# Optimization experiments

Hardware: AMD Instinct MI355X
Metric: run time of the kernel (lower is better)

## Reference

```python
import jax, jax.numpy as jnp
import numpy as np

DEPTH = 2   # depth
H = 8       # heads
DH = 32     # dim_head
DIM = 256   # model dim (= H*DH)
W = 2       # sliding_window_size
C = 4       # compress_block_size == selection_block_size
NSEL = 2    # num_selected_blocks
B, S = 4, 2048


def layernorm(x, g, b, eps=1e-5):
    m = x.mean(-1, keepdims=True)
    v = jnp.var(x, axis=-1, keepdims=True)
    return (x - m) * jax.lax.rsqrt(v + eps) * g + b


def msoftmax(s, mask):
    # numerically-safe masked softmax; rows with no visible key output zeros
    s = jnp.where(mask, s, -1e9)
    p = jax.nn.softmax(s, axis=-1)
    return jnp.where(jnp.any(mask, axis=-1, keepdims=True), p, 0.0)


def nsa(x, Wq, Wk, Wv, Wg, Wo):
    # Native sparse attention: compressed + top-k selected blocks + sliding window,
    # combined with per-head sigmoid gates.
    b, s, d = x.shape
    nb = s // C
    q = (x @ Wq).reshape(b, s, H, DH).transpose(0, 2, 1, 3)  # [B,H,S,DH]
    k = (x @ Wk).reshape(b, s, H, DH).transpose(0, 2, 1, 3)
    v = (x @ Wv).reshape(b, s, H, DH).transpose(0, 2, 1, 3)
    scale = DH ** -0.5
    t = jnp.arange(s)

    # ---- compressed branch: mean-pooled KV blocks, causal over fully-past blocks
    kb = k.reshape(b, H, nb, C, DH)
    vb = v.reshape(b, H, nb, C, DH)
    kc = kb.mean(3)
    vc = vb.mean(3)
    sc = jnp.einsum('bhsd,bhnd->bhsn', q, kc) * scale       # [B,H,S,nb]
    blk_end = jnp.arange(nb) * C + (C - 1)
    cmask = blk_end[None, :] <= t[:, None]                   # [S,nb]
    pc = msoftmax(sc, cmask[None, None])
    oc = jnp.einsum('bhsn,bhnd->bhsd', pc, vc)

    # ---- selection branch: own block always + top (NSEL-1) blocks by compressed score
    own = t // C                                             # [S]
    not_own = jnp.arange(nb)[None, :] != own[:, None]        # [S,nb]
    sel_scores = jnp.where(not_own[None, None], pc, -1.0)
    top_idx = jax.lax.top_k(sel_scores, NSEL - 1)[1]         # [B,H,S,NSEL-1]
    own_idx = jnp.broadcast_to(own[None, None, :, None], (b, H, s, 1))
    idx = jnp.concatenate([own_idx, top_idx], axis=-1)       # [B,H,S,NSEL]
    idxf = idx.reshape(b, H, s * NSEL, 1, 1)
    sk = jnp.take_along_axis(kb, idxf, axis=2).reshape(b, H, s, NSEL * C, DH)
    sv = jnp.take_along_axis(vb, idxf, axis=2).reshape(b, H, s, NSEL * C, DH)
    pos = (idx[..., None] * C + jnp.arange(C)).reshape(b, H, s, NSEL * C)
    fmask = pos <= t[None, None, :, None]
    sf = jnp.einsum('bhsd,bhskd->bhsk', q, sk) * scale
    pf = msoftmax(sf, fmask)
    of = jnp.einsum('bhsk,bhskd->bhsd', pf, sv)

    # ---- sliding-window branch: causal local window of W tokens (incl. self)
    off = jnp.arange(W) - (W - 1)
    wpos = t[:, None] + off[None, :]                         # [S,W]
    widx = jnp.clip(wpos, 0, s - 1)
    kw = jnp.take(k, widx.reshape(-1), axis=2).reshape(b, H, s, W, DH)
    vw = jnp.take(v, widx.reshape(-1), axis=2).reshape(b, H, s, W, DH)
    sw = jnp.einsum('bhsd,bhsjd->bhsj', q, kw) * scale
    pw = msoftmax(sw, (wpos >= 0)[None, None])
    ow = jnp.einsum('bhsj,bhsjd->bhsd', pw, vw)

    # ---- gated combine + output projection
    g = jax.nn.sigmoid(x @ Wg).reshape(b, s, 3, H).transpose(0, 3, 1, 2)  # [B,H,S,3]
    o = g[..., 0:1] * oc + g[..., 1:2] * of + g[..., 2:3] * ow
    return o.transpose(0, 2, 1, 3).reshape(b, s, H * DH) @ Wo


def forward(x, ln_a_g, ln_a_b, Wq, Wk, Wv, Wg, Wo, ln_f_g, ln_f_b, W1, b1, W2, b2):
    for l in range(DEPTH):
        for j in range(2):  # two attention sub-layers per block
            i = l * 2 + j
            h = layernorm(x, ln_a_g[i], ln_a_b[i])
            x = x + nsa(h, Wq[i], Wk[i], Wv[i], Wg[i], Wo[i])
        h = layernorm(x, ln_f_g[l], ln_f_b[l])
        h = h @ W1[l] + b1[l]
        h = jnp.where(h > 0, h, 0.01 * h)  # LeakyReLU
        x = x + h @ W2[l] + b2[l]
    return x


def setup_inputs() -> dict:
    key = jax.random.key(0)
    ks = jax.random.split(key, 8)
    A = DEPTH * 2
    r = lambda k, shp: jax.random.normal(k, shp, jnp.float32) * 0.02
    return {
        'x': jax.random.normal(ks[0], (B, S, DIM), jnp.float32),
        'ln_a_g': jnp.ones((A, DIM), jnp.float32),
        'ln_a_b': jnp.zeros((A, DIM), jnp.float32),
        'Wq': r(ks[1], (A, DIM, H * DH)),
        'Wk': r(ks[2], (A, DIM, H * DH)),
        'Wv': r(ks[3], (A, DIM, H * DH)),
        'Wg': r(ks[4], (A, DIM, 3 * H)),
        'Wo': r(ks[5], (A, H * DH, DIM)),
        'ln_f_g': jnp.ones((DEPTH, DIM), jnp.float32),
        'ln_f_b': jnp.zeros((DEPTH, DIM), jnp.float32),
        'W1': r(ks[6], (DEPTH, DIM, 2 * DIM)),
        'b1': jnp.zeros((DEPTH, 2 * DIM), jnp.float32),
        'W2': r(ks[7], (DEPTH, 2 * DIM, DIM)),
        'b2': jnp.zeros((DEPTH, DIM), jnp.float32),
    }


def reference(x, ln_a_g, ln_a_b, Wq, Wk, Wv, Wg, Wo, ln_f_g, ln_f_b, W1, b1, W2, b2):
    return forward(x, ln_a_g, ln_a_b, Wq, Wk, Wv, Wg, Wo, ln_f_g, ln_f_b, W1, b1, W2, b2)
```

## Files before the change

### kernel.cpp

```cpp
#include <hip/hip_runtime.h>
#include <hip/hip_bf16.h>
#include <math.h>

#define NH 8
#define DH 32
#define DIM 256
#define SEQ 2048
#define BATCH 4
#define NB 512
#define QKS 512
#define VGS 320
#define SCALE 0.17677669529663687f

typedef short short8v __attribute__((ext_vector_type(8)));
typedef float float4v __attribute__((ext_vector_type(4)));

__device__ __forceinline__ float sigmoidf_(float x){ return 1.f/(1.f+__expf(-x)); }
__device__ __forceinline__ ushort f2bf(float f){
  uint b = __float_as_uint(f);
  return (ushort)((b + 0x7fffu + ((b>>16)&1u)) >> 16);
}
__device__ __forceinline__ float bf2f(ushort u){ return __uint_as_float(((uint)u)<<16); }
__device__ __forceinline__ float bflo(uint u){ return __uint_as_float(u<<16); }
__device__ __forceinline__ float bfhi(uint u){ return __uint_as_float(u & 0xffff0000u); }
__device__ __forceinline__ uint pk2(float a, float b){ return (uint)f2bf(a) | ((uint)f2bf(b)<<16); }
__device__ __forceinline__ void bfu4_to_f32(uint4 u, float* f){
  f[0]=bflo(u.x); f[1]=bfhi(u.x);
  f[2]=bflo(u.y); f[3]=bfhi(u.y);
  f[4]=bflo(u.z); f[5]=bfhi(u.z);
  f[6]=bflo(u.w); f[7]=bfhi(u.w);
}

__global__ void copy_f32(const float* __restrict__ in, float* __restrict__ out, int n4){
  int i = blockIdx.x*blockDim.x + threadIdx.x;
  if (i < n4) ((float4*)out)[i] = ((const float4*)in)[i];
}

__global__ void build_wqk(const float* __restrict__ Wq, const float* __restrict__ Wk, float* __restrict__ out){
  int i = blockIdx.x*256 + threadIdx.x;
  if (i >= 4*256*QKS) return;
  int col = i & 511, rk = (i>>9)&255, l = i>>17;
  out[i] = (col < 256) ? Wq[((size_t)l*256+rk)*256+col] : Wk[((size_t)l*256+rk)*256+col-256];
}
__global__ void build_wvgT(const float* __restrict__ Wv, const float* __restrict__ Wg, ushort* __restrict__ out){
  int i = blockIdx.x*256 + threadIdx.x;
  if (i >= 4*VGS*256) return;
  int k = i & 255, n = (i>>8)%VGS, l = i/(VGS*256);
  float v = 0.f;
  if      (n < 256) v = Wv[((size_t)l*256+k)*256+n];
  else if (n < 280) v = Wg[((size_t)l*256+k)*24 + (n-256)];
  out[i] = f2bf(v);
}
__global__ void build_wT(const float* __restrict__ in, ushort* __restrict__ out, int L, int K, int N){
  int i = blockIdx.x*256 + threadIdx.x;
  if (i >= L*K*N) return;
  int k = i % K, n = (i/K) % N, l = i/(K*N);
  out[i] = f2bf(in[((size_t)l*K+k)*N+n]);
}

__global__ __launch_bounds__(256) void ln_k(const float* __restrict__ x, const float* __restrict__ g,
                                            const float* __restrict__ b, float* __restrict__ h,
                                            ushort* __restrict__ hb){
  int row  = blockIdx.x*4 + (threadIdx.x>>6);
  int lane = threadIdx.x & 63;
  int c = lane*4;
  const float* xr = x + (size_t)row*DIM + c;
  float4 v = *(const float4*)xr;
  float s = v.x+v.y+v.z+v.w;
  float q = v.x*v.x+v.y*v.y+v.z*v.z+v.w*v.w;
  #pragma unroll
  for (int off=32; off>0; off>>=1){ s += __shfl_xor(s, off); q += __shfl_xor(q, off); }
  float mean = s * (1.f/DIM);
  float var  = q * (1.f/DIM) - mean*mean;
  float rs = rsqrtf(var + 1e-5f);
  float4 gg = *(const float4*)(g + c);
  float4 bb = *(const float4*)(b + c);
  float4 o;
  o.x = (v.x-mean)*rs*gg.x + bb.x;
  o.y = (v.y-mean)*rs*gg.y + bb.y;
  o.z = (v.z-mean)*rs*gg.z + bb.z;
  o.w = (v.w-mean)*rs*gg.w + bb.w;
  *(float4*)(h + (size_t)row*DIM + c) = o;
  uint2 u;
  u.x = pk2(o.x, o.y);
  u.y = pk2(o.z, o.w);
  *(uint2*)&hb[(size_t)row*DIM + c] = u;
}

template<bool BIAS, bool LEAKY, bool ACC>
__global__ __launch_bounds__(256) void gemm_f32(const float* __restrict__ A, const float* __restrict__ B,
                                                const float* __restrict__ bias, float* __restrict__ C,
                                                int M, int N, int K){
  __shared__ float As[32][132];
  __shared__ float Bs[32][68];
  int tid = threadIdx.x;
  int m0 = blockIdx.x*128, n0 = blockIdx.y*64;
  int tx = tid & 15, ty = tid >> 4;
  int ar = tid >> 1;
  int ac = (tid & 1)*16;
  int bk = tid >> 3;
  int bn = (tid & 7)*8;
  const float* Ap = A + (size_t)(m0+ar)*K + ac;
  const float* Bp = B + (size_t)bk*N + n0 + bn;
  float4 apre[4], bpre[2];
  #pragma unroll
  for (int j=0;j<4;j++) apre[j] = *(const float4*)(Ap + 4*j);
  bpre[0] = *(const float4*)Bp;
  bpre[1] = *(const float4*)(Bp + 4);
  float acc[8][4];
  #pragma unroll
  for (int i=0;i<8;i++)
    #pragma unroll
    for (int j=0;j<4;j++) acc[i][j]=0.f;
  for (int k0=0; k0<K; k0+=32){
    #pragma unroll
    for (int j=0;j<4;j++){
      As[ac+4*j+0][ar]=apre[j].x; As[ac+4*j+1][ar]=apre[j].y;
      As[ac+4*j+2][ar]=apre[j].z; As[ac+4*j+3][ar]=apre[j].w;
    }
    *(float4*)&Bs[bk][bn]   = bpre[0];
    *(float4*)&Bs[bk][bn+4] = bpre[1];
    __syncthreads();
    if (k0 + 32 < K){
      #pragma unroll
      for (int j=0;j<4;j++) apre[j] = *(const float4*)(Ap + k0 + 32 + 4*j);
      bpre[0] = *(const float4*)(Bp + (size_t)(k0+32)*N);
      bpre[1] = *(const float4*)(Bp + (size_t)(k0+32)*N + 4);
    }
    #pragma unroll
    for (int kk=0;kk<32;kk++){
      float4 bv  = *(const float4*)&Bs[kk][tx*4];
      float4 av0 = *(const float4*)&As[kk][ty*8];
      float4 av1 = *(const float4*)&As[kk][ty*8+4];
      float av[8] = {av0.x,av0.y,av0.z,av0.w,av1.x,av1.y,av1.z,av1.w};
      float bw[4] = {bv.x,bv.y,bv.z,bv.w};
      #pragma unroll
      for (int i=0;i<8;i++)
        #pragma unroll
        for (int j=0;j<4;j++) acc[i][j] += av[i]*bw[j];
    }
    __syncthreads();
  }
  #pragma unroll
  for (int i=0;i<8;i++){
    int m = m0 + ty*8 + i;
    #pragma unroll
    for (int j=0;j<4;j++){
      int n = n0 + tx*4 + j;
      float val = acc[i][j];
      if (BIAS)  val += bias[n];
      if (LEAKY) val = val > 0.f ? val : 0.01f*val;
      float* cp = C + (size_t)m*N + n;
      if (ACC) val += *cp;
      *cp = val;
    }
  }
}

template<bool BIAS, bool LEAKY, bool ACC, bool OBF16>
__global__ __launch_bounds__(256) void gemm_bf16(const ushort* __restrict__ A, const ushort* __restrict__ Bt,
                                                 const float* __restrict__ bias, void* __restrict__ Cv,
                                                 int M, int N, int K){
  __shared__ ushort Al[128*64];
  __shared__ ushort Bl[64*64];
  int tid = threadIdx.x;
  int m0 = blockIdx.x*128, n0 = blockIdx.y*64;
  int w = tid>>6, lane = tid&63;
  int wm = w>>1, wn = w&1;
  float4v acc[4][2];
  #pragma unroll
  for (int i=0;i<4;i++)
    #pragma unroll
    for (int j=0;j<2;j++) acc[i][j] = (float4v){0.f,0.f,0.f,0.f};
  for (int k0=0; k0<K; k0+=64){
    #pragma unroll
    for (int i=0;i<4;i++){
      int id = tid + 256*i;
      int r = id>>3, c = id&7;
      *(uint4*)&Al[r*64 + ((c ^ (r&7))*8)] = *(const uint4*)&A[(size_t)(m0+r)*K + k0 + c*8];
    }
    #pragma unroll
    for (int i=0;i<2;i++){
      int id = tid + 256*i;
      int r = id>>3, c = id&7;
      *(uint4*)&Bl[r*64 + ((c ^ (r&7))*8)] = *(const uint4*)&Bt[(size_t)(n0+r)*K + k0 + c*8];
    }
    __syncthreads();
    #pragma unroll
    for (int kk=0; kk<2; ++kk){
      short8v a[4], bfr[2];
      #pragma unroll
      for (int mf=0; mf<4; mf++){
        int r = wm*64 + mf*16 + (lane&15);
        int c = (kk*4 + (lane>>4)) ^ (r&7);
        a[mf] = *(short8v*)&Al[r*64 + c*8];
      }
      #pragma unroll
      for (int nf=0; nf<2; nf++){
        int r = wn*32 + nf*16 + (lane&15);
        int c = (kk*4 + (lane>>4)) ^ (r&7);
        bfr[nf] = *(short8v*)&Bl[r*64 + c*8];
      }
      #pragma unroll
      for (int mf=0; mf<4; mf++)
        #pragma unroll
        for (int nf=0; nf<2; nf++)
          acc[mf][nf] = __builtin_amdgcn_mfma_f32_16x16x32_bf16(a[mf], bfr[nf], acc[mf][nf], 0, 0, 0);
    }
    __syncthreads();
  }
  #pragma unroll
  for (int nf=0; nf<2; nf++){
    int col = n0 + wn*32 + nf*16 + (lane&15);
    float bv = BIAS ? bias[col] : 0.f;
    #pragma unroll
    for (int mf=0; mf<4; mf++){
      #pragma unroll
      for (int r=0; r<4; r++){
        int row = m0 + wm*64 + mf*16 + (lane>>4)*4 + r;
        float vv = acc[mf][nf][r];
        if (BIAS) vv += bv;
        if (LEAKY) vv = vv > 0.f ? vv : 0.01f*vv;
        if (OBF16) ((ushort*)Cv)[(size_t)row*N + col] = f2bf(vv);
        else {
          float* C = (float*)Cv;
          if (ACC) vv += C[(size_t)row*N + col];
          C[(size_t)row*N + col] = vv;
        }
      }
    }
  }
}

__global__ void pool_k(const float* __restrict__ qk, const ushort* __restrict__ vg,
                       float* __restrict__ kc, ushort* __restrict__ vc){
  int i = blockIdx.x*256 + threadIdx.x;
  if (i >= BATCH*NH*NB*DH) return;
  int d = i & 31, n = (i >> 5) & 511, h = (i >> 14) & 7, b = i >> 17;
  size_t kb = ((size_t)(b*SEQ + n*4))*QKS + 256 + h*DH + d;
  kc[i] = 0.25f*(qk[kb] + qk[kb+QKS] + qk[kb+2*QKS] + qk[kb+3*QKS]);
  size_t vb = ((size_t)(b*SEQ + n*4))*VGS + h*DH + d;
  vc[i] = f2bf(0.25f*(bf2f(vg[vb]) + bf2f(vg[vb+VGS]) + bf2f(vg[vb+2*VGS]) + bf2f(vg[vb+3*VGS])));
}

__global__ __launch_bounds__(256, 4) void nsa_attn(
    const float* __restrict__ qk, const ushort* __restrict__ vg,
    const float* __restrict__ kc, const ushort* __restrict__ vc,
    ushort* __restrict__ o)
{
  __shared__ float  kt[64*32];
  __shared__ ushort vt[64*32];
  __shared__ ushort accs[4*64*32];
  __shared__ float4 meta[4*64];
  int e = blockIdx.x;
  int hh = e & 7;
  int b  = (e >> 3) & 3;
  int qq = (e >> 5) & 7;
  int r  = e >> 8;
  int g  = (r==0) ? (31-qq) : (r==1) ? qq : (r==2) ? (23-qq) : (8+qq);
  int tid = threadIdx.x;
  int w = tid >> 6, lane = tid & 63;
  const float*  kcg = kc + ((size_t)(b*NH + hh)*NB)*DH;
  const ushort* vcg = vc + ((size_t)(b*NH + hh)*NB)*DH;

  {
    int t = g*64 + lane;
    int own = t >> 2, nvis = (t+1) >> 2;
    int nmax = 16*(g+1);
    float qv[32];
    {
      const float4* qr = (const float4*)(qk + ((size_t)b*SEQ + t)*QKS + hh*DH);
      #pragma unroll
      for (int d8=0; d8<8; d8++){
        float4 a4 = qr[d8];
        qv[4*d8]=a4.x; qv[4*d8+1]=a4.y; qv[4*d8+2]=a4.z; qv[4*d8+3]=a4.w;
      }
    }
    float l = 0.f, best = -1e30f;
    int bn1 = -1;
    float acc[32];
    #pragma unroll
    for (int d=0;d<32;d++) acc[d]=0.f;

    int tiles = (g + 4) >> 2;
    for (int ti=0; ti<tiles; ++ti){
      int base = ti*64;
      if (ti) __syncthreads();
      {
        const float4* sk = (const float4*)(kcg + (size_t)base*DH);
        const uint4*  sv = (const uint4*)(vcg + (size_t)base*DH);
        ((float4*)kt)[tid]     = sk[tid];
        ((float4*)kt)[tid+256] = sk[tid+256];
        ((uint4*)vt)[tid]      = sv[tid];
      }
      __syncthreads();
      int jmax = (nmax - base - w + 3) >> 2;
      if (jmax > 16) jmax = 16;
      for (int j=0; j<jmax; ++j){
        int rr = w + 4*j;
        int n = base + rr;
        const float4* kp = (const float4*)&kt[rr*32];
        float s = 0.f;
        #pragma unroll
        for (int d8=0; d8<8; d8++){
          float4 k4 = kp[d8];
          s += qv[4*d8]*k4.x + qv[4*d8+1]*k4.y + qv[4*d8+2]*k4.z + qv[4*d8+3]*k4.w;
        }
        s *= SCALE;
        bool act = (n < nvis);
        if (act && n != own && s > best){ best = s; bn1 = n; }
        float p = act ? __expf(s) : 0.f;
        l += p;
        const uint4* vp = (const uint4*)&vt[rr*32];
        #pragma unroll
        for (int q4=0; q4<4; ++q4){
          uint4 u = vp[q4];
          float f[8]; bfu4_to_f32(u, f);
          #pragma unroll
          for (int z=0; z<8; z++) acc[8*q4+z] += p*f[z];
        }
      }
    }
    ushort* pr = &accs[((size_t)w*64 + lane)*32];
    #pragma unroll
    for (int q8=0; q8<4; q8++){
      uint4 u;
      u.x = pk2(acc[8*q8+0],acc[8*q8+1]); u.y = pk2(acc[8*q8+2],acc[8*q8+3]);
      u.z = pk2(acc[8*q8+4],acc[8*q8+5]); u.w = pk2(acc[8*q8+6],acc[8*q8+7]);
      *(uint4*)&pr[q8*8] = u;
    }
    meta[w*64 + lane] = make_float4(l, best, __int_as_float(bn1), 0.f);
  }
  __syncthreads();

  {
    int tok = tid >> 2;
    int ds  = (tid & 3)*8;
    int t = g*64 + tok;
    int own = t >> 2, nvis = (t+1) >> 2;
    float q8[8];
    {
      const float4* qr = (const float4*)(qk + ((size_t)b*SEQ + t)*QKS + hh*DH + ds);
      float4 a4 = qr[0], b4 = qr[1];
      q8[0]=a4.x; q8[1]=a4.y; q8[2]=a4.z; q8[3]=a4.w;
      q8[4]=b4.x; q8[5]=b4.y; q8[6]=b4.z; q8[7]=b4.w;
    }
    float out8[8];
    #pragma unroll
    for (int j=0;j<8;j++) out8[j]=0.f;
    float ll = 0.f, bb = -1e30f;
    int bn = (own==0) ? 1 : 0;
    #pragma unroll
    for (int sp=0; sp<4; ++sp){
      uint4 u = *(const uint4*)&accs[((size_t)sp*64 + tok)*32 + ds];
      float f[8]; bfu4_to_f32(u, f);
      #pragma unroll
      for (int j=0;j<8;j++) out8[j] += f[j];
      float4 m4 = meta[sp*64 + tok];
      ll += m4.x;
      int mi = __float_as_int(m4.z);
      if (m4.y > bb || (m4.y == bb && mi >= 0 && mi < bn)){ bb = m4.y; bn = mi; }
    }
    const ushort* gr = vg + ((size_t)b*SEQ + t)*VGS + 256;
    float g0 = sigmoidf_(bf2f(gr[hh])), g1 = sigmoidf_(bf2f(gr[8+hh])), g2 = sigmoidf_(bf2f(gr[16+hh]));
    float inv = (nvis > 0) ? g0/ll : 0.f;
    #pragma unroll
    for (int j=0;j<8;j++) out8[j] *= inv;

    const float*  kb2 = qk + (size_t)b*SEQ*QKS + 256 + hh*DH + ds;
    const ushort* vb2 = vg + (size_t)b*SEQ*VGS + hh*DH + ds;
    float s2[8];
    float m2 = -1e30f;
    #pragma unroll
    for (int ki=0; ki<8; ++ki){
      int tt = (ki<4 ? own : bn)*4 + (ki&3);
      float s = -1e30f;
      if (tt <= t){
        const float4* kr = (const float4*)(kb2 + (size_t)tt*QKS);
        float4 a4 = kr[0], c4 = kr[1];
        float ps = q8[0]*a4.x + q8[1]*a4.y + q8[2]*a4.z + q8[3]*a4.w
                 + q8[4]*c4.x + q8[5]*c4.y + q8[6]*c4.z + q8[7]*c4.w;
        ps += __shfl_xor(ps, 1);
        ps += __shfl_xor(ps, 2);
        s = ps*SCALE;
        m2 = fmaxf(m2, s);
      }
      s2[ki] = s;
    }
    float l2 = 0.f;
    #pragma unroll
    for (int ki=0; ki<8; ++ki)
      if (s2[ki] > -1e29f) l2 += __expf(s2[ki] - m2);
    float inv2 = g1/l2;
    #pragma unroll
    for (int ki=0; ki<8; ++ki){
      int tt = (ki<4 ? own : bn)*4 + (ki&3);
      if (tt <= t){
        float pw = __expf(s2[ki] - m2) * inv2;
        uint4 u = *(const uint4*)(vb2 + (size_t)tt*VGS);
        float f[8]; bfu4_to_f32(u, f);
        #pragma unroll
        for (int j=0;j<8;j++) out8[j] += pw*f[j];
      }
    }

    int tp = (t>0) ? t-1 : 0;
    float sa, sb;
    {
      const float4* ka = (const float4*)(kb2 + (size_t)tp*QKS);
      const float4* kb4= (const float4*)(kb2 + (size_t)t *QKS);
      float4 a0 = ka[0], a1 = ka[1], b0 = kb4[0], b1 = kb4[1];
      float pa_ = q8[0]*a0.x + q8[1]*a0.y + q8[2]*a0.z + q8[3]*a0.w
                + q8[4]*a1.x + q8[5]*a1.y + q8[6]*a1.z + q8[7]*a1.w;
      float pb_ = q8[0]*b0.x + q8[1]*b0.y + q8[2]*b0.z + q8[3]*b0.w
                + q8[4]*b1.x + q8[5]*b1.y + q8[6]*b1.z + q8[7]*b1.w;
      pa_ += __shfl_xor(pa_, 1); pa_ += __shfl_xor(pa_, 2);
      pb_ += __shfl_xor(pb_, 1); pb_ += __shfl_xor(pb_, 2);
      sa = pa_*SCALE; sb = pb_*SCALE;
    }
    float m3 = (t>0) ? fmaxf(sa, sb) : sb;
    float pa = (t>0) ? __expf(sa-m3) : 0.f;
    float pb = __expf(sb-m3);
    float inv3 = g2/(pa+pb);
    float va[8], vbv[8];
    bfu4_to_f32(*(const uint4*)(vb2 + (size_t)tp*VGS), va);
    bfu4_to_f32(*(const uint4*)(vb2 + (size_t)t *VGS), vbv);
    ushort* orow = o + ((size_t)b*SEQ + t)*DIM + hh*DH + ds;
    float rr[8];
    #pragma unroll
    for (int j=0;j<8;j++) rr[j] = out8[j] + (pa*va[j] + pb*vbv[j])*inv3;
    uint4 u;
    u.x = pk2(rr[0], rr[1]);
    u.y = pk2(rr[2], rr[3]);
    u.z = pk2(rr[4], rr[5]);
    u.w = pk2(rr[6], rr[7]);
    *(uint4*)orow = u;
  }
}

extern "C" void kernel_launch(void* const* d_in, const int* in_sizes, int n_in,
                              void* d_out, int out_size, void* d_ws, size_t ws_size,
                              hipStream_t stream) {
  const float* x_in   = (const float*)d_in[0];
  const float* ln_a_g = (const float*)d_in[1];
  const float* ln_a_b = (const float*)d_in[2];
  const float* Wq     = (const float*)d_in[3];
  const float* Wk     = (const float*)d_in[4];
  const float* Wv     = (const float*)d_in[5];
  const float* Wg     = (const float*)d_in[6];
  const float* Wo     = (const float*)d_in[7];
  const float* ln_f_g = (const float*)d_in[8];
  const float* ln_f_b = (const float*)d_in[9];
  const float* W1     = (const float*)d_in[10];
  const float* b1     = (const float*)d_in[11];
  const float* W2     = (const float*)d_in[12];
  const float* b2     = (const float*)d_in[13];

  float* xout = (float*)d_out;
  float* ws = (float*)d_ws;
  const size_t NTOK = (size_t)BATCH*SEQ;
  float* h    = ws;
  float* qkb  = h    + NTOK*DIM;
  float* kcb  = qkb  + NTOK*QKS;
  ushort* vcb = (ushort*)(kcb + (size_t)BATCH*NH*NB*DH);
  float* wqk  = (float*)(vcb + (size_t)BATCH*NH*NB*DH);
  ushort* hb   = (ushort*)(wqk + (size_t)4*DIM*QKS);
  ushort* vgu  = hb   + NTOK*DIM;
  ushort* obu  = vgu  + NTOK*VGS;
  ushort* midu = obu  + NTOK*DIM;
  ushort* wvgT = midu + NTOK*512;
  ushort* woT  = wvgT + (size_t)4*VGS*DIM;
  ushort* w1T  = woT  + (size_t)4*DIM*DIM;
  ushort* w2T  = w1T  + (size_t)2*512*DIM;

  copy_f32<<<2048, 256, 0, stream>>>(x_in, xout, (int)(NTOK*DIM/4));
  build_wqk <<<(4*256*QKS+255)/256, 256, 0, stream>>>(Wq, Wk, wqk);
  build_wvgT<<<(4*VGS*256+255)/256, 256, 0, stream>>>(Wv, Wg, wvgT);
  build_wT  <<<(4*256*256+255)/256, 256, 0, stream>>>(Wo, woT, 4, 256, 256);
  build_wT  <<<(2*256*512+255)/256, 256, 0, stream>>>(W1, w1T, 2, 256, 512);
  build_wT  <<<(2*512*256+255)/256, 256, 0, stream>>>(W2, w2T, 2, 512, 256);

  dim3 gqk(64,8), gvg(64,5), g4(64,4), g8(64,8);
  for (int i=0;i<4;i++){
    ln_k<<<2048,256,0,stream>>>(xout, ln_a_g + i*DIM, ln_a_b + i*DIM, h, hb);
    gemm_f32<false,false,false><<<gqk,256,0,stream>>>(h, wqk + (size_t)i*DIM*QKS, nullptr, qkb, 8192,QKS,256);
    gemm_bf16<false,false,false,true><<<gvg,256,0,stream>>>(hb, wvgT + (size_t)i*VGS*DIM, nullptr, vgu, 8192,VGS,256);
    pool_k<<<2048,256,0,stream>>>(qkb, vgu, kcb, vcb);
    nsa_attn<<<1024,256,0,stream>>>(qkb, vgu, kcb, vcb, obu);
    gemm_bf16<false,false,true,false><<<g4,256,0,stream>>>(obu, woT + (size_t)i*DIM*DIM, nullptr, xout, 8192,DIM,256);
    if (i & 1){
      int l = i >> 1;
      ln_k<<<2048,256,0,stream>>>(xout, ln_f_g + l*DIM, ln_f_b + l*DIM, h, hb);
      gemm_bf16<true,true,false,true><<<g8,256,0,stream>>>(hb,   w1T + (size_t)l*512*DIM, b1 + l*512, midu, 8192,512,256);
      gemm_bf16<true,false,true,false><<<g4,256,0,stream>>>(midu, w2T + (size_t)l*DIM*512, b2 + l*DIM, xout, 8192,DIM,512);
    }
  }
}
```

Measured before the change: 611.4 us.

## Compute compressed-branch P·V with bf16 MFMA using transposed pooled values

The pooling kernel now writes the compressed value blocks transposed (dim-major), and the attention kernel stages bf16 probabilities in shared memory. The P·V product for the compressed branch then runs as 16x16x32 bf16 MFMA instructions instead of per-thread scalar FMAs over 32 dims. This also changes the score work split: each wave now handles a contiguous 16-key slice instead of strided keys, and the four per-wave partial accumulators no longer need a cross-wave reduction. The cost is an extra barrier per tile and probabilities rounded to bf16 before accumulation.

```diff
diff --git a/kernel.cpp b/kernel.cpp
--- a/kernel.cpp
+++ b/kernel.cpp
@@ -233,24 +233,26 @@
 }
 
 __global__ void pool_k(const float* __restrict__ qk, const ushort* __restrict__ vg,
-                       float* __restrict__ kc, ushort* __restrict__ vc){
+                       float* __restrict__ kc, ushort* __restrict__ vct){
   int i = blockIdx.x*256 + threadIdx.x;
   if (i >= BATCH*NH*NB*DH) return;
   int d = i & 31, n = (i >> 5) & 511, h = (i >> 14) & 7, b = i >> 17;
   size_t kb = ((size_t)(b*SEQ + n*4))*QKS + 256 + h*DH + d;
   kc[i] = 0.25f*(qk[kb] + qk[kb+QKS] + qk[kb+2*QKS] + qk[kb+3*QKS]);
   size_t vb = ((size_t)(b*SEQ + n*4))*VGS + h*DH + d;
-  vc[i] = f2bf(0.25f*(bf2f(vg[vb]) + bf2f(vg[vb+VGS]) + bf2f(vg[vb+2*VGS]) + bf2f(vg[vb+3*VGS])));
+  float pv = 0.25f*(bf2f(vg[vb]) + bf2f(vg[vb+VGS]) + bf2f(vg[vb+2*VGS]) + bf2f(vg[vb+3*VGS]));
+  vct[(((size_t)(b*NH + h))*DH + d)*NB + n] = f2bf(pv);
 }
 
 __global__ __launch_bounds__(256, 4) void nsa_attn(
     const float* __restrict__ qk, const ushort* __restrict__ vg,
-    const float* __restrict__ kc, const ushort* __restrict__ vc,
+    const float* __restrict__ kc, const ushort* __restrict__ vct,
     ushort* __restrict__ o)
 {
   __shared__ float  kt[64*32];
-  __shared__ ushort vt[64*32];
-  __shared__ ushort accs[4*64*32];
+  __shared__ ushort vcT[32*72];
+  __shared__ ushort Pl[64*72];
+  __shared__ float  ocl[64*36];
   __shared__ float4 meta[4*64];
   int e = blockIdx.x;
   int hh = e & 7;
@@ -260,8 +262,8 @@
   int g  = (r==0) ? (31-qq) : (r==1) ? qq : (r==2) ? (23-qq) : (8+qq);
   int tid = threadIdx.x;
   int w = tid >> 6, lane = tid & 63;
-  const float*  kcg = kc + ((size_t)(b*NH + hh)*NB)*DH;
-  const ushort* vcg = vc + ((size_t)(b*NH + hh)*NB)*DH;
+  const float*  kcg  = kc  + ((size_t)(b*NH + hh)*NB)*DH;
+  const ushort* vctg = vct + ((size_t)(b*NH + hh)*DH)*NB;
 
   {
     int t = g*64 + lane;
@@ -278,9 +280,8 @@
     }
     float l = 0.f, best = -1e30f;
     int bn1 = -1;
-    float acc[32];
-    #pragma unroll
-    for (int d=0;d<32;d++) acc[d]=0.f;
+    float4v acc0 = (float4v){0.f,0.f,0.f,0.f};
+    float4v acc1 = (float4v){0.f,0.f,0.f,0.f};
 
     int tiles = (g + 4) >> 2;
     for (int ti=0; ti<tiles; ++ti){
@@ -288,46 +289,58 @@
       if (ti) __syncthreads();
       {
         const float4* sk = (const float4*)(kcg + (size_t)base*DH);
-        const uint4*  sv = (const uint4*)(vcg + (size_t)base*DH);
         ((float4*)kt)[tid]     = sk[tid];
         ((float4*)kt)[tid+256] = sk[tid+256];
-        ((uint4*)vt)[tid]      = sv[tid];
+        int sd = tid >> 3, sn = (tid & 7)*8;
+        *(uint4*)&vcT[sd*72 + sn] = *(const uint4*)&vctg[(size_t)sd*NB + base + sn];
       }
       __syncthreads();
-      int jmax = (nmax - base - w + 3) >> 2;
-      if (jmax > 16) jmax = 16;
-      for (int j=0; j<jmax; ++j){
-        int rr = w + 4*j;
+      float ps[16];
+      #pragma unroll
+      for (int j=0; j<16; ++j){
+        int rr = w*16 + j;
         int n = base + rr;
-        const float4* kp = (const float4*)&kt[rr*32];
-        float s = 0.f;
-        #pragma unroll
-        for (int d8=0; d8<8; d8++){
-          float4 k4 = kp[d8];
-          s += qv[4*d8]*k4.x + qv[4*d8+1]*k4.y + qv[4*d8+2]*k4.z + qv[4*d8+3]*k4.w;
+        float p = 0.f;
+        if (n < nmax){
+          const float4* kp = (const float4*)&kt[rr*32];
+          float s = 0.f;
+          #pragma unroll
+          for (int d8=0; d8<8; d8++){
+            float4 k4 = kp[d8];
+            s += qv[4*d8]*k4.x + qv[4*d8+1]*k4.y + qv[4*d8+2]*k4.z + qv[4*d8+3]*k4.w;
+          }
+          s *= SCALE;
+          bool act = (n < nvis);
+          if (act && n != own && s > best){ best = s; bn1 = n; }
+          p = act ? __expf(s) : 0.f;
+          l += p;
         }
-        s *= SCALE;
-        bool act = (n < nvis);
-        if (act && n != own && s > best){ best = s; bn1 = n; }
-        float p = act ? __expf(s) : 0.f;
-        l += p;
-        const uint4* vp = (const uint4*)&vt[rr*32];
-        #pragma unroll
-        for (int q4=0; q4<4; ++q4){
-          uint4 u = vp[q4];
-          float f[8]; bfu4_to_f32(u, f);
-          #pragma unroll
-          for (int z=0; z<8; z++) acc[8*q4+z] += p*f[z];
-        }
-      }
-    }
-    ushort* pr = &accs[((size_t)w*64 + lane)*32];
-    #pragma unroll
-    for (int q8=0; q8<4; q8++){
-      uint4 u;
-      u.x = pk2(acc[8*q8+0],acc[8*q8+1]); u.y = pk2(acc[8*q8+2],acc[8*q8+3]);
-      u.z = pk2(acc[8*q8+4],acc[8*q8+5]); u.w = pk2(acc[8*q8+6],acc[8*q8+7]);
-      *(uint4*)&pr[q8*8] = u;
+        ps[j] = p;
+      }
+      {
+        uint4 u0, u1;
+        u0.x = pk2(ps[0],ps[1]);  u0.y = pk2(ps[2],ps[3]);
+        u0.z = pk2(ps[4],ps[5]);  u0.w = pk2(ps[6],ps[7]);
+        u1.x = pk2(ps[8],ps[9]);  u1.y = pk2(ps[10],ps[11]);
+        u1.z = pk2(ps[12],ps[13]);u1.w = pk2(ps[14],ps[15]);
+        *(uint4*)&Pl[lane*72 + w*16]     = u0;
+        *(uint4*)&Pl[lane*72 + w*16 + 8] = u1;
+      }
+      __syncthreads();
+      #pragma unroll
+      for (int ks=0; ks<2; ++ks){
+        short8v a  = *(short8v*)&Pl [(16*w + (lane&15))*72 + ks*32 + (lane>>4)*8];
+        short8v b0 = *(short8v*)&vcT[(lane&15)*72        + ks*32 + (lane>>4)*8];
+        short8v b1 = *(short8v*)&vcT[((lane&15)+16)*72   + ks*32 + (lane>>4)*8];
+        acc0 = __builtin_amdgcn_mfma_f32_16x16x32_bf16(a, b0, acc0, 0, 0, 0);
+        acc1 = __builtin_amdgcn_mfma_f32_16x16x32_bf16(a, b1, acc1, 0, 0, 0);
+      }
+    }
+    #pragma unroll
+    for (int r2=0; r2<4; ++r2){
+      int token = 16*w + (lane>>4)*4 + r2;
+      ocl[token*36 + (lane&15)]      = acc0[r2];
+      ocl[token*36 + 16 + (lane&15)] = acc1[r2];
     }
     meta[w*64 + lane] = make_float4(l, best, __int_as_float(bn1), 0.f);
   }
@@ -346,16 +359,16 @@
       q8[4]=b4.x; q8[5]=b4.y; q8[6]=b4.z; q8[7]=b4.w;
     }
     float out8[8];
-    #pragma unroll
-    for (int j=0;j<8;j++) out8[j]=0.f;
+    {
+      float4 oA = *(const float4*)&ocl[tok*36 + ds];
+      float4 oB = *(const float4*)&ocl[tok*36 + ds + 4];
+      out8[0]=oA.x; out8[1]=oA.y; out8[2]=oA.z; out8[3]=oA.w;
+      out8[4]=oB.x; out8[5]=oB.y; out8[6]=oB.z; out8[7]=oB.w;
+    }
     float ll = 0.f, bb = -1e30f;
     int bn = (own==0) ? 1 : 0;
     #pragma unroll
     for (int sp=0; sp<4; ++sp){
-      uint4 u = *(const uint4*)&accs[((size_t)sp*64 + tok)*32 + ds];
-      float f[8]; bfu4_to_f32(u, f);
-      #pragma unroll
-      for (int j=0;j<8;j++) out8[j] += f[j];
       float4 m4 = meta[sp*64 + tok];
       ll += m4.x;
       int mi = __float_as_int(m4.z);
@@ -462,8 +475,8 @@
   float* h    = ws;
   float* qkb  = h    + NTOK*DIM;
   float* kcb  = qkb  + NTOK*QKS;
-  ushort* vcb = (ushort*)(kcb + (size_t)BATCH*NH*NB*DH);
-  float* wqk  = (float*)(vcb + (size_t)BATCH*NH*NB*DH);
+  ushort* vctb = (ushort*)(kcb + (size_t)BATCH*NH*NB*DH);
+  float* wqk  = (float*)(vctb + (size_t)BATCH*NH*NB*DH);
   ushort* hb   = (ushort*)(wqk + (size_t)4*DIM*QKS);
   ushort* vgu  = hb   + NTOK*DIM;
   ushort* obu  = vgu  + NTOK*VGS;
@@ -485,8 +498,8 @@
     ln_k<<<2048,256,0,stream>>>(xout, ln_a_g + i*DIM, ln_a_b + i*DIM, h, hb);
     gemm_f32<false,false,false><<<gqk,256,0,stream>>>(h, wqk + (size_t)i*DIM*QKS, nullptr, qkb, 8192,QKS,256);
     gemm_bf16<false,false,false,true><<<gvg,256,0,stream>>>(hb, wvgT + (size_t)i*VGS*DIM, nullptr, vgu, 8192,VGS,256);
-    pool_k<<<2048,256,0,stream>>>(qkb, vgu, kcb, vcb);
-    nsa_attn<<<1024,256,0,stream>>>(qkb, vgu, kcb, vcb, obu);
+    pool_k<<<2048,256,0,stream>>>(qkb, vgu, kcb, vctb);
+    nsa_attn<<<1024,256,0,stream>>>(qkb, vgu, kcb, vctb, obu);
     gemm_bf16<false,false,true,false><<<g4,256,0,stream>>>(obu, woT + (size_t)i*DIM*DIM, nullptr, xout, 8192,DIM,256);
     if (i & 1){
       int l = i >> 1;
```

Measured after the change: 543.1 us, median of 2. 1.13x faster.
